# Kernel optimization log

Hardware: AMD Instinct MI355X
Metric: run time of the kernel (lower is better)

## Reference

```python
import jax, jax.numpy as jnp
import numpy as np

XZ = jnp.array([0, 2])
XY = jnp.array([0, 1])
YZ = jnp.array([1, 2])


def _bilinear(plane, uv):
    """plane: (C,R,R) as (C,H,W); uv: (N,2) in [0,1], uv[:,0]->width, uv[:,1]->height.
    Border padding + align_corners=True semantics (grid_sample style)."""
    R = plane.shape[-1]
    xy = jnp.clip(uv, 0.0, 1.0) * (R - 1)
    x, y = xy[:, 0], xy[:, 1]
    x0 = jnp.floor(x)
    y0 = jnp.floor(y)
    x0i = jnp.clip(x0.astype(jnp.int32), 0, R - 1)
    y0i = jnp.clip(y0.astype(jnp.int32), 0, R - 1)
    x1i = jnp.clip(x0i + 1, 0, R - 1)
    y1i = jnp.clip(y0i + 1, 0, R - 1)
    wx = (x - x0)[None, :]  # (1,N)
    wy = (y - y0)[None, :]
    f00 = plane[:, y0i, x0i]  # (C,N)
    f01 = plane[:, y0i, x1i]
    f10 = plane[:, y1i, x0i]
    f11 = plane[:, y1i, x1i]
    top = f00 * (1.0 - wx) + f01 * wx
    bot = f10 * (1.0 - wx) + f11 * wx
    return (top * (1.0 - wy) + bot * wy).T  # (N,C)


def _sample_triplane(p, c_xz, c_xy, c_yz):
    """p: (bs,N,3) in [0,1]; planes: (bs,C,R,R). Returns (bs,N,C) summed over planes."""
    def per_batch(pb, fxz, fxy, fyz):
        return (_bilinear(fxz, pb[:, XZ])
                + _bilinear(fxy, pb[:, XY])
                + _bilinear(fyz, pb[:, YZ]))
    return jax.vmap(per_batch)(p, c_xz, c_xy, c_yz)


def setup_inputs() -> dict:
    key = jax.random.key(0)
    ks = jax.random.split(key, 12)
    bs, ns, C, S, R = 2, 50000, 32, 8, 128
    inp = {
        "query_pos": jax.random.uniform(ks[0], (bs, ns, 3), dtype=jnp.float32),
        "c_xz": jax.random.normal(ks[1], (bs, C, R, R), dtype=jnp.float32),
        "c_xy": jax.random.normal(ks[2], (bs, C, R, R), dtype=jnp.float32),
        "c_yz": jax.random.normal(ks[3], (bs, C, R, R), dtype=jnp.float32),
        # offset weights scaled small so sampled points stay mostly in-bounds
        "W_off": jax.random.normal(ks[4], (C, S * 3), dtype=jnp.float32) * 0.01,
        "b_off": jnp.zeros((S * 3,), dtype=jnp.float32),
        "W_w": jax.random.normal(ks[5], (C, S), dtype=jnp.float32) * 0.1,
        "b_w": jnp.zeros((S,), dtype=jnp.float32),
        "W_v": jax.random.normal(ks[6], (C, C), dtype=jnp.float32) * (1.0 / np.sqrt(C)),
        "b_v": jnp.zeros((C,), dtype=jnp.float32),
        "W_out": jax.random.normal(ks[7], (C, C), dtype=jnp.float32) * (1.0 / np.sqrt(C)),
        "b_out": jnp.zeros((C,), dtype=jnp.float32),
    }
    return inp


def reference(query_pos, c_xz, c_xy, c_yz, W_off, b_off, W_w, b_w, W_v, b_v, W_out, b_out):
    bs, ns, _ = query_pos.shape
    S = W_w.shape[1]
    # round 1: sample tri-plane features at query points
    feature = _sample_triplane(query_pos, c_xz, c_xy, c_yz)  # (bs,ns,C)
    # predict per-query sample offsets and weights
    off = (feature @ W_off + b_off).reshape(bs, ns, S, 3)
    w = (feature @ W_w + b_w).reshape(bs, ns, S, 1)
    pts = off + query_pos[:, :, None, :]  # (bs,ns,S,3)
    # round 2: sample at deformed points
    aux = _sample_triplane(pts.reshape(bs, ns * S, 3), c_xz, c_xy, c_yz)
    v = aux.reshape(bs, ns, S, -1) @ W_v + b_v  # (bs,ns,S,C)
    out = (v * w).sum(-2)                        # weighted reduce over samples
    out = out @ W_out + b_out + feature          # residual
    return out  # (bs,ns,C)
```

## Files before the change

kernel.cpp:

```cpp
#include <hip/hip_runtime.h>
#include <hip/hip_fp16.h>

#define BS 2
#define NS 50000
#define CCH 32
#define RR 128
#define SS 8

typedef float v2f __attribute__((ext_vector_type(2)));


__global__ __launch_bounds__(256)
void prep(const float* __restrict__ cxz,
          const float* __restrict__ cxy,
          const float* __restrict__ cyz,
          const float* __restrict__ Wv, const float* __restrict__ bv,
          const float* __restrict__ Wout,
          unsigned short* __restrict__ tp, float* __restrict__ Wc,
          float* __restrict__ bvw) {
    __shared__ float lds[32 * 129];
    int tid = threadIdx.x;
    int row = blockIdx.x;
    if (row < BS * 3 * RR) {
        int y  = row & 127;
        int pl = (row >> 7) % 3;
        int b  = row / 384;
        const float* src = (pl == 0) ? cxz : ((pl == 1) ? cxy : cyz);
        const float* sp = src + (((size_t)(b * CCH)) << 14) + (y << 7);
#pragma unroll
        for (int i = 0; i < 16; ++i) {
            int c = (tid >> 7) + 2 * i;
            int x = tid & 127;
            lds[c * 129 + x] = sp[((size_t)c << 14) + x];
        }
        __syncthreads();
        ushort2* dst = (ushort2*)(tp + ((size_t)row << 12));
#pragma unroll
        for (int i = 0; i < 8; ++i) {
            int c2 = tid & 15;
            int x  = (tid >> 4) + 16 * i;
            ushort2 v;
            v.x = __half_as_ushort(__float2half(lds[(2 * c2) * 129 + x]));
            v.y = __half_as_ushort(__float2half(lds[(2 * c2 + 1) * 129 + x]));
            dst[(x << 4) + c2] = v;
        }
    } else {
        int t = (row - BS * 3 * RR) * 256 + tid;
        int c = t >> 5, j = t & 31;
        float acc = 0.f;
#pragma unroll
        for (int k = 0; k < 32; ++k) acc += Wv[c * 32 + k] * Wout[k * 32 + j];
        Wc[t] = acc;
        if (t < 32) {
            float a2 = 0.f;
#pragma unroll
            for (int k = 0; k < 32; ++k) a2 += bv[k] * Wout[k * 32 + t];
            bvw[t] = a2;
        }
    }
}


struct f8 { v2f a[4]; };

__device__ __forceinline__ void acc8(f8& acc, uint4 u, float w) {
    __half2 h0 = __builtin_bit_cast(__half2, u.x);
    __half2 h1 = __builtin_bit_cast(__half2, u.y);
    __half2 h2 = __builtin_bit_cast(__half2, u.z);
    __half2 h3 = __builtin_bit_cast(__half2, u.w);
    acc.a[0].x = fmaf(__half2float(h0.x), w, acc.a[0].x);
    acc.a[0].y = fmaf(__half2float(h0.y), w, acc.a[0].y);
    acc.a[1].x = fmaf(__half2float(h1.x), w, acc.a[1].x);
    acc.a[1].y = fmaf(__half2float(h1.y), w, acc.a[1].y);
    acc.a[2].x = fmaf(__half2float(h2.x), w, acc.a[2].x);
    acc.a[2].y = fmaf(__half2float(h2.y), w, acc.a[2].y);
    acc.a[3].x = fmaf(__half2float(h3.x), w, acc.a[3].x);
    acc.a[3].y = fmaf(__half2float(h3.y), w, acc.a[3].y);
}

__device__ __forceinline__ void axq(float p, int& i0, int& i1, float& w) {
    float x = fminf(fmaxf(p, 0.f), 1.f) * 127.f;
    float f = floorf(x);
    i0 = (int)f;
    i1 = min(i0 + 1, 127);
    w = x - f;
}

__device__ __forceinline__ void plane_acc(f8& acc, const uint4* __restrict__ P,
                                          int xi0, int xi1, float wx,
                                          int yi0, int yi1, float wy) {
    int r0 = yi0 << 9, r1 = yi1 << 9;
    int c0 = xi0 << 2, c1 = xi1 << 2;
    uint4 u00 = P[r0 + c0];
    uint4 u01 = P[r0 + c1];
    uint4 u10 = P[r1 + c0];
    uint4 u11 = P[r1 + c1];
    float w11 = wx * wy;
    float w01 = wx - w11;
    float w10 = wy - w11;
    float w00 = 1.f - wx - w10;
    acc8(acc, u00, w00);
    acc8(acc, u01, w01);
    acc8(acc, u10, w10);
    acc8(acc, u11, w11);
}

__device__ __forceinline__ void sample3(f8& acc, const uint4* __restrict__ P0,
                                        float p0, float p1, float p2) {
    int a0i0, a0i1, a1i0, a1i1, a2i0, a2i1;
    float w0, w1, w2;
    axq(p0, a0i0, a0i1, w0);
    axq(p1, a1i0, a1i1, w1);
    axq(p2, a2i0, a2i1, w2);
    plane_acc(acc, P0,             a0i0, a0i1, w0, a2i0, a2i1, w2);
    plane_acc(acc, P0 + (1 << 16), a0i0, a0i1, w0, a1i0, a1i1, w1);
    plane_acc(acc, P0 + (2 << 16), a1i0, a1i1, w1, a2i0, a2i1, w2);
}

#define GETE(v, idx) (((idx) & 1) ? (v).a[((idx) >> 1) & 3].y : (v).a[((idx) >> 1) & 3].x)
#define GETC(v, idx) __shfl(GETE(v, idx), base | ((idx) >> 3), 64)

__global__ __launch_bounds__(128)
void eda_main(const float* __restrict__ qp, const unsigned short* __restrict__ tp,
              const float* __restrict__ Woff, const float* __restrict__ boff,
              const float* __restrict__ Ww, const float* __restrict__ bw,
              const float* __restrict__ Wc, const float* __restrict__ bvw,
              const float* __restrict__ bout, float* __restrict__ out) {
    __shared__ v2f sWcat[32][4][4];
    __shared__ v2f sWc[32][4][4];
    __shared__ float sbcat[32];
    __shared__ float sbvw[32];
    __shared__ float sbout[32];

    int tid = threadIdx.x;
    for (int i = tid; i < 1024; i += 128) {
        int k = i >> 5, j = i & 31;
        ((float*)sWcat)[i] = (j < 24) ? Woff[k * 24 + j] : Ww[k * 8 + (j - 24)];
        ((float*)sWc)[i]   = Wc[i];
    }
    if (tid < 32) {
        sbcat[tid] = (tid < 24) ? boff[tid] : bw[tid - 24];
        sbvw[tid]  = bvw[tid];
        sbout[tid] = bout[tid];
    }
    __syncthreads();

    int lane = tid & 3;
    int base = tid & 60;
    int b  = blockIdx.x & 1;
    int qi = (blockIdx.x >> 1) * 32 + (tid >> 2);
    int qq = min(qi, NS - 1);

    const float* p = qp + ((size_t)b * NS + qq) * 3;
    float p0 = p[0], p1 = p[1], p2 = p[2];

    const uint4* P0 = (const uint4*)tp + (((size_t)(b * 3)) << 16) + lane;

    f8 feat = {};
    sample3(feat, P0, p0, p1, p2);

    f8 cat;
#pragma unroll
    for (int e = 0; e < 4; ++e) {
        cat.a[e].x = sbcat[(lane << 3) + 2 * e];
        cat.a[e].y = sbcat[(lane << 3) + 2 * e + 1];
    }
#pragma unroll
    for (int k = 0; k < 32; ++k) {
        float fc = GETC(feat, k);
        v2f fc2 = {fc, fc};
#pragma unroll
        for (int e = 0; e < 4; ++e)
            cat.a[e] = __builtin_elementwise_fma(fc2, sWcat[k][lane][e], cat.a[e]);
    }

    float w_s[SS], o0[SS], o1[SS], o2[SS];
#pragma unroll
    for (int s = 0; s < SS; ++s) {
        w_s[s] = GETC(cat, 24 + s);
        o0[s]  = GETC(cat, 3 * s + 0);
        o1[s]  = GETC(cat, 3 * s + 1);
        o2[s]  = GETC(cat, 3 * s + 2);
    }

    f8 wa = {};
    float wsum = 0.f;
#pragma unroll
    for (int s = 0; s < SS; ++s) {
        f8 aux = {};
        sample3(aux, P0, p0 + o0[s], p1 + o1[s], p2 + o2[s]);
        v2f w2 = {w_s[s], w_s[s]};
#pragma unroll
        for (int e = 0; e < 4; ++e)
            wa.a[e] = __builtin_elementwise_fma(w2, aux.a[e], wa.a[e]);
        wsum += w_s[s];
    }

    f8 o;
    v2f ws2 = {wsum, wsum};
#pragma unroll
    for (int e = 0; e < 4; ++e) {
        v2f bo  = {sbout[(lane << 3) + 2 * e], sbout[(lane << 3) + 2 * e + 1]};
        v2f bv2 = {sbvw[(lane << 3) + 2 * e], sbvw[(lane << 3) + 2 * e + 1]};
        o.a[e] = __builtin_elementwise_fma(ws2, bv2, bo) + feat.a[e];
    }
#pragma unroll
    for (int k = 0; k < 32; ++k) {
        float wc = GETC(wa, k);
        v2f wc2 = {wc, wc};
#pragma unroll
        for (int e = 0; e < 4; ++e)
            o.a[e] = __builtin_elementwise_fma(wc2, sWc[k][lane][e], o.a[e]);
    }

    if (qi < NS) {
        float* dst = out + ((size_t)b * NS + qi) * 32 + (lane << 3);
        *(float4*)dst       = make_float4(o.a[0].x, o.a[0].y, o.a[1].x, o.a[1].y);
        *(float4*)(dst + 4) = make_float4(o.a[2].x, o.a[2].y, o.a[3].x, o.a[3].y);
    }
}

extern "C" void kernel_launch(void* const* d_in, const int* in_sizes, int n_in,
                              void* d_out, int out_size, void* d_ws, size_t ws_size,
                              hipStream_t stream) {
    const float* qp   = (const float*)d_in[0];
    const float* cxz  = (const float*)d_in[1];
    const float* cxy  = (const float*)d_in[2];
    const float* cyz  = (const float*)d_in[3];
    const float* Woff = (const float*)d_in[4];
    const float* boff = (const float*)d_in[5];
    const float* Ww   = (const float*)d_in[6];
    const float* bw   = (const float*)d_in[7];
    const float* Wv   = (const float*)d_in[8];
    const float* bv   = (const float*)d_in[9];
    const float* Wout = (const float*)d_in[10];
    const float* bout = (const float*)d_in[11];
    float* out = (float*)d_out;

    unsigned short* tp = (unsigned short*)d_ws;
    float* Wc  = (float*)((char*)d_ws + (size_t)BS * 3 * RR * RR * CCH * 2);
    float* bvw = Wc + 1024;

    prep<<<BS * 3 * RR + 4, 256, 0, stream>>>(cxz, cxy, cyz, Wv, bv, Wout, tp, Wc, bvw);
    int blocks_per_batch = (NS + 31) / 32;
    eda_main<<<2 * blocks_per_batch, 128, 0, stream>>>(qp, tp, Woff, boff, Ww, bw,
                                                       Wc, bvw, bout, out);
}
```

Measured before the change: 138.3 us.

## Software-pipeline triplane gathers and overlap first gather with weight staging

Splits each triplane sample into a load phase that issues all 12 gathers and a separate evaluate phase. The gathers for the next deformed sample are issued before the current one is evaluated, a double-buffered pipeline. The first-round gather is also issued before the shared-memory weight staging and barrier so its latency overlaps that setup. This hides gather latency in exchange for more live registers (24 uint4 in flight), which may lower occupancy.

```diff
diff --git a/kernel.cpp b/kernel.cpp
--- a/kernel.cpp
+++ b/kernel.cpp
@@ -63,6 +63,8 @@
 
 struct f8 { v2f a[4]; };
 
+struct Samp { uint4 u[12]; float f0, f1, f2; };
+
 __device__ __forceinline__ void acc8(f8& acc, uint4 u, float w) {
     __half2 h0 = __builtin_bit_cast(__half2, u.x);
     __half2 h1 = __builtin_bit_cast(__half2, u.y);
@@ -86,35 +88,45 @@
     w = x - f;
 }
 
-__device__ __forceinline__ void plane_acc(f8& acc, const uint4* __restrict__ P,
-                                          int xi0, int xi1, float wx,
-                                          int yi0, int yi1, float wy) {
-    int r0 = yi0 << 9, r1 = yi1 << 9;
-    int c0 = xi0 << 2, c1 = xi1 << 2;
-    uint4 u00 = P[r0 + c0];
-    uint4 u01 = P[r0 + c1];
-    uint4 u10 = P[r1 + c0];
-    uint4 u11 = P[r1 + c1];
+__device__ __forceinline__ Samp load_samp(const uint4* __restrict__ P0,
+                                          float p0, float p1, float p2) {
+    Samp t;
+    int i00, i01, i10, i11, i20, i21;
+    axq(p0, i00, i01, t.f0);
+    axq(p1, i10, i11, t.f1);
+    axq(p2, i20, i21, t.f2);
+    const uint4* Pxz = P0;
+    const uint4* Pxy = P0 + (1 << 16);
+    const uint4* Pyz = P0 + (2 << 16);
+    int c00 = i00 << 2, c01 = i01 << 2;
+    int c10 = i10 << 2, c11 = i11 << 2;
+    int r10 = i10 << 9, r11 = i11 << 9;
+    int r20 = i20 << 9, r21 = i21 << 9;
+    t.u[0]  = Pxz[r20 + c00];  t.u[1]  = Pxz[r20 + c01];
+    t.u[2]  = Pxz[r21 + c00];  t.u[3]  = Pxz[r21 + c01];
+    t.u[4]  = Pxy[r10 + c00];  t.u[5]  = Pxy[r10 + c01];
+    t.u[6]  = Pxy[r11 + c00];  t.u[7]  = Pxy[r11 + c01];
+    t.u[8]  = Pyz[r20 + c10];  t.u[9]  = Pyz[r20 + c11];
+    t.u[10] = Pyz[r21 + c10];  t.u[11] = Pyz[r21 + c11];
+    return t;
+}
+
+__device__ __forceinline__ void eval_plane(f8& acc, const uint4* u,
+                                           float wx, float wy) {
     float w11 = wx * wy;
     float w01 = wx - w11;
     float w10 = wy - w11;
     float w00 = 1.f - wx - w10;
-    acc8(acc, u00, w00);
-    acc8(acc, u01, w01);
-    acc8(acc, u10, w10);
-    acc8(acc, u11, w11);
-}
-
-__device__ __forceinline__ void sample3(f8& acc, const uint4* __restrict__ P0,
-                                        float p0, float p1, float p2) {
-    int a0i0, a0i1, a1i0, a1i1, a2i0, a2i1;
-    float w0, w1, w2;
-    axq(p0, a0i0, a0i1, w0);
-    axq(p1, a1i0, a1i1, w1);
-    axq(p2, a2i0, a2i1, w2);
-    plane_acc(acc, P0,             a0i0, a0i1, w0, a2i0, a2i1, w2);
-    plane_acc(acc, P0 + (1 << 16), a0i0, a0i1, w0, a1i0, a1i1, w1);
-    plane_acc(acc, P0 + (2 << 16), a1i0, a1i1, w1, a2i0, a2i1, w2);
+    acc8(acc, u[0], w00);
+    acc8(acc, u[1], w01);
+    acc8(acc, u[2], w10);
+    acc8(acc, u[3], w11);
+}
+
+__device__ __forceinline__ void eval_samp(const Samp& t, f8& acc) {
+    eval_plane(acc, t.u + 0, t.f0, t.f2);
+    eval_plane(acc, t.u + 4, t.f0, t.f1);
+    eval_plane(acc, t.u + 8, t.f1, t.f2);
 }
 
 #define GETE(v, idx) (((idx) & 1) ? (v).a[((idx) >> 1) & 3].y : (v).a[((idx) >> 1) & 3].x)
@@ -133,18 +145,6 @@
     __shared__ float sbout[32];
 
     int tid = threadIdx.x;
-    for (int i = tid; i < 1024; i += 128) {
-        int k = i >> 5, j = i & 31;
-        ((float*)sWcat)[i] = (j < 24) ? Woff[k * 24 + j] : Ww[k * 8 + (j - 24)];
-        ((float*)sWc)[i]   = Wc[i];
-    }
-    if (tid < 32) {
-        sbcat[tid] = (tid < 24) ? boff[tid] : bw[tid - 24];
-        sbvw[tid]  = bvw[tid];
-        sbout[tid] = bout[tid];
-    }
-    __syncthreads();
-
     int lane = tid & 3;
     int base = tid & 60;
     int b  = blockIdx.x & 1;
@@ -156,8 +156,22 @@
 
     const uint4* P0 = (const uint4*)tp + (((size_t)(b * 3)) << 16) + lane;
 
+    Samp fs = load_samp(P0, p0, p1, p2);
+
+    for (int i = tid; i < 1024; i += 128) {
+        int k = i >> 5, j = i & 31;
+        ((float*)sWcat)[i] = (j < 24) ? Woff[k * 24 + j] : Ww[k * 8 + (j - 24)];
+        ((float*)sWc)[i]   = Wc[i];
+    }
+    if (tid < 32) {
+        sbcat[tid] = (tid < 24) ? boff[tid] : bw[tid - 24];
+        sbvw[tid]  = bvw[tid];
+        sbout[tid] = bout[tid];
+    }
+    __syncthreads();
+
     f8 feat = {};
-    sample3(feat, P0, p0, p1, p2);
+    eval_samp(fs, feat);
 
     f8 cat;
 #pragma unroll
@@ -174,26 +188,28 @@
             cat.a[e] = __builtin_elementwise_fma(fc2, sWcat[k][lane][e], cat.a[e]);
     }
 
-    float w_s[SS], o0[SS], o1[SS], o2[SS];
-#pragma unroll
-    for (int s = 0; s < SS; ++s) {
-        w_s[s] = GETC(cat, 24 + s);
-        o0[s]  = GETC(cat, 3 * s + 0);
-        o1[s]  = GETC(cat, 3 * s + 1);
-        o2[s]  = GETC(cat, 3 * s + 2);
-    }
-
     f8 wa = {};
     float wsum = 0.f;
+    float w_cur = GETC(cat, 24);
+    Samp cur = load_samp(P0, p0 + GETC(cat, 0), p1 + GETC(cat, 1), p2 + GETC(cat, 2));
+    Samp nxt;
+    float w_nxt;
 #pragma unroll
     for (int s = 0; s < SS; ++s) {
+        if (s < SS - 1) {
+            w_nxt = GETC(cat, 24 + (s + 1));
+            nxt = load_samp(P0, p0 + GETC(cat, 3 * (s + 1) + 0),
+                                p1 + GETC(cat, 3 * (s + 1) + 1),
+                                p2 + GETC(cat, 3 * (s + 1) + 2));
+        }
         f8 aux = {};
-        sample3(aux, P0, p0 + o0[s], p1 + o1[s], p2 + o2[s]);
-        v2f w2 = {w_s[s], w_s[s]};
+        eval_samp(cur, aux);
+        v2f w2 = {w_cur, w_cur};
 #pragma unroll
         for (int e = 0; e < 4; ++e)
             wa.a[e] = __builtin_elementwise_fma(w2, aux.a[e], wa.a[e]);
-        wsum += w_s[s];
+        wsum += w_cur;
+        if (s < SS - 1) { cur = nxt; w_cur = w_nxt; }
     }
 
     f8 o;
```

Measured after the change: 139.1 us. No clear change (+0.6%).
